# Optimization experiments

Measured on AMD Instinct MI355X. Metric: run time of the kernel, lower is better.

The kernel has to match this reference:

```python
import jax, jax.numpy as jnp
import numpy as np

ATTN_WINDOW = 7  # attention_window from attn_params; dilation (attention_stride) = 1


def _xavier(key, shape):
    lim = np.sqrt(6.0 / (shape[0] + shape[1]))
    return jax.random.uniform(key, shape, jnp.float32, -lim, lim)


def setup_inputs() -> dict:
    key = jax.random.key(0)
    ks = jax.random.split(key, 8)
    B, Cin, Him, Wim = 4, 3, 112, 112
    Cmid, Cout = 128, 128
    x = jax.random.normal(ks[0], (B, Cin, Him, Wim), jnp.float32)
    conv_w = jax.random.normal(ks[1], (Cmid, Cin, 3, 3), jnp.float32) * 0.1  # OIHW
    conv_b = jnp.zeros((Cmid,), jnp.float32)
    q_w = _xavier(ks[2], (Cmid, Cmid)); q_b = jnp.zeros((Cmid,), jnp.float32)
    k_w = _xavier(ks[3], (Cmid, Cmid)); k_b = jnp.zeros((Cmid,), jnp.float32)
    v_w = _xavier(ks[4], (Cout, Cmid)); v_b = jnp.zeros((Cout,), jnp.float32)
    return {"x": x, "conv_w": conv_w, "conv_b": conv_b,
            "q_w": q_w, "q_b": q_b, "k_w": k_w, "k_b": k_b, "v_w": v_w, "v_b": v_b}


def _neighbor_idx(n, ksz):
    # NATTEN-style neighborhood: centered window, clamped to stay inside the image.
    starts = jnp.clip(jnp.arange(n) - ksz // 2, 0, n - ksz)
    return starts[:, None] + jnp.arange(ksz)[None, :]  # [n, ksz]


def reference(x, conv_w, conv_b, q_w, q_b, k_w, k_b, v_w, v_b):
    # conv stem (3x3, stride 2, pad 1) + ReLU
    f = jax.lax.conv_general_dilated(
        x, conv_w, window_strides=(2, 2), padding=[(1, 1), (1, 1)],
        dimension_numbers=("NCHW", "OIHW", "NCHW"))
    f = jax.nn.relu(f + conv_b[None, :, None, None])
    f = f.transpose(0, 2, 3, 1)  # NHWC  [B,H,W,Cmid]
    # 1x1 convs == per-pixel linear layers
    q = f @ q_w.T + q_b
    k = f @ k_w.T + k_b
    v = f @ v_w.T + v_b
    B, H, W, C = q.shape
    ksz = min(ATTN_WINDOW, H, W)
    ksz -= 1 if ksz % 2 == 0 else 0
    ih = _neighbor_idx(H, ksz)  # [H, ksz]
    iw = _neighbor_idx(W, ksz)  # [W, ksz]
    # gather per-pixel neighborhoods: [B,H,W,ksz,ksz,C]
    kn = k[:, ih[:, None, :, None], iw[None, :, None, :], :]
    vn = v[:, ih[:, None, :, None], iw[None, :, None, :], :]
    scale = C ** -0.5
    logits = jnp.einsum("bhwc,bhwijc->bhwij", q * scale, kn)
    attn = jax.nn.softmax(logits.reshape(B, H, W, -1), axis=-1).reshape(logits.shape)
    out = jnp.einsum("bhwij,bhwijc->bhwc", attn, vn)  # [B,H,W,Cout]
    return out.transpose(0, 3, 1, 2)  # back to NCHW
```

## Files before the change

### kernel.cpp

```cpp
#include <hip/hip_runtime.h>
#include <hip/hip_bf16.h>
#include <math.h>

#define HW 56
#define PPI (HW*HW)
#define NB 4
#define C 128
#define NPIX (NB*PPI)

typedef __attribute__((ext_vector_type(8))) short short8;
typedef __attribute__((ext_vector_type(4))) float f32x4;

__device__ __forceinline__ short bfbits(float v) {
    __hip_bfloat16 hb = __float2bfloat16(v);
    return *reinterpret_cast<short*>(&hb);
}
__device__ __forceinline__ unsigned packbf(float a, float b) {
    return (unsigned)(unsigned short)bfbits(a) | ((unsigned)(unsigned short)bfbits(b) << 16);
}

__global__ __launch_bounds__(256) void prep_kernel(
    const float* __restrict__ cw,
    const float* __restrict__ qw, const float* __restrict__ kw,
    const float* __restrict__ vw,
    __hip_bfloat16* __restrict__ wcf, __hip_bfloat16* __restrict__ wqkv)
{
    int gid = blockIdx.x * 256 + threadIdx.x;
    if (blockIdx.x < 192) {
        int m   = gid >> 14;
        int r   = gid & 16383;
        int col = r >> 7;
        int k   = r & 127;
        const float* W = (m == 0) ? qw : (m == 1) ? kw : vw;
        int kk = k >> 5, hi = (k >> 3) & 3, j = k & 7;
        wqkv[m * 16384 + ((kk * 4 + hi) * 128 + col) * 8 + j] = __float2bfloat16(W[col * 128 + k]);
    } else {
        int idx = gid - 192 * 256;
        int hi = idx >> 10, cout = (idx >> 3) & 127, j = idx & 7;
        int k  = hi * 8 + j;
        float v = (k < 27) ? cw[cout * 27 + k] : 0.f;
        wcf[(hi * 128 + cout) * 8 + j] = __float2bfloat16(v);
    }
}

#define VPITCH 272
#define XPITCH 24
#define XCH    504
#define LPITCH 100

__global__ __launch_bounds__(256, 2) void fused_kernel(
    const float* __restrict__ x, const __hip_bfloat16* __restrict__ wcf,
    const float* __restrict__ cb, const __hip_bfloat16* __restrict__ wqkv,
    const float* __restrict__ qb, const float* __restrict__ kb,
    const float* __restrict__ vb, float* __restrict__ out)
{
    __shared__ __align__(16) short vT[128 * 136];
    __shared__ __align__(16) short poolA[4][16 * 128];
    __shared__ __align__(16) short poolB[16 * 136];
    __shared__ __align__(16) float logit_s[16 * LPITCH];
    short* q_lds = poolA[0];
    short* x_lds = poolB;
    short* attnW = poolB;

    int t = threadIdx.x, lane = t & 63, wid = t >> 6;
    int r16 = lane & 15, hi = lane >> 4;

    int bx = blockIdx.x;
    int b  = bx / 196;
    int rr = bx % 196;
    int th = rr / 14, tw = rr % 14;
    int ih0 = min(max(th*4 - 3, 0), HW - 10);
    int iw0 = min(max(tw*4 - 3, 0), HW - 10);

    {
        int ihA = 2*ih0 - 1, iwA = 2*iw0 - 1;
        #pragma unroll
        for (int it = 0; it < 6; ++it) {
            int i = t + 256*it;
            if (i < 1512) {
                int ci = i / XCH, r = i % XCH;
                int row = r / XPITCH, col = r % XPITCH;
                int ih = ihA + row, iw = iwA + col;
                float xv = 0.f;
                if (col < 21 && ih >= 0 && ih < 112 && iw >= 0 && iw < 112)
                    xv = x[((size_t)(b*3 + ci)*112 + ih)*112 + iw];
                x_lds[i] = bfbits(xv);
            }
        }
    }

    for (int i = t; i < 1024; i += 256) {
        int c = i >> 3, j = i & 7;
        int hsw = (c >> 3) & 7;
        int unit = (14 + (j >> 2)) ^ hsw;
        *(unsigned*)((char*)vT + c*VPITCH + (unit << 4) + (j & 3)*4) = 0u;
    }

    int  offb[8];
    bool vmask[8];
    #pragma unroll
    for (int j = 0; j < 8; ++j) {
        int k = hi*8 + j;
        int ci = k/9, r9 = k%9, kh = r9/3, kw_ = r9%3;
        offb[j]  = ci*XCH + kh*XPITCH + kw_;
        vmask[j] = (k < 27);
    }
    float qbias[2];
    #pragma unroll
    for (int i = 0; i < 2; ++i) qbias[i] = qb[(wid*2 + i)*16 + r16];

    __syncthreads();

    short8 qa[4];
    {
        int cout0 = (wid*2 + 0)*16 + r16;
        int cout1 = (wid*2 + 1)*16 + r16;
        short8 cbw0 = *(const short8*)((const short*)wcf + (hi*128 + cout0)*8);
        short8 cbw1 = *(const short8*)((const short*)wcf + (hi*128 + cout1)*8);
        float cbias0 = cb[cout0], cbias1 = cb[cout1];

        int ph = th*4 + (r16 >> 2), pw = tw*4 + (r16 & 3);
        int hl = ph - ih0, wl = pw - iw0;
        int pb = hl*(2*XPITCH) + wl*2;
        short8 af;
        #pragma unroll
        for (int j = 0; j < 8; ++j)
            af[j] = vmask[j] ? x_lds[offb[j] + pb] : (short)0;
        #pragma unroll
        for (int ctl = 0; ctl < 2; ++ctl) {
            int cout   = ctl ? cout1  : cout0;
            short8 bw  = ctl ? cbw1   : cbw0;
            float bias = ctl ? cbias1 : cbias0;
            f32x4 acc = {0.f, 0.f, 0.f, 0.f};
            acc = __builtin_amdgcn_mfma_f32_16x16x32_bf16(af, bw, acc, 0, 0, 0);
            int colblk = cout >> 3, inb = (cout & 7)*2;
            #pragma unroll
            for (int rg = 0; rg < 4; ++rg) {
                int px = hi*4 + rg;
                *(short*)((char*)q_lds + px*256 + ((colblk ^ px) << 4) + inb)
                    = bfbits(fmaxf(acc[rg] + bias, 0.f));
            }
        }
        __syncthreads();

        short8 fa[4];
        #pragma unroll
        for (int kk = 0; kk < 4; ++kk)
            fa[kk] = *(const short8*)((char*)q_lds + r16*256 + (((kk*4 + hi) ^ r16) << 4));

        __syncthreads();

        #pragma unroll
        for (int i = 0; i < 2; ++i) {
            int ct = wid*2 + i;
            const short* wb = (const short*)wqkv + hi*1024 + r16*8 + ct*128;
            f32x4 acc = {0.f, 0.f, 0.f, 0.f};
            acc = __builtin_amdgcn_mfma_f32_16x16x32_bf16(fa[0], *(const short8*)(wb),         acc, 0, 0, 0);
            acc = __builtin_amdgcn_mfma_f32_16x16x32_bf16(fa[1], *(const short8*)(wb +  4096), acc, 0, 0, 0);
            acc = __builtin_amdgcn_mfma_f32_16x16x32_bf16(fa[2], *(const short8*)(wb +  8192), acc, 0, 0, 0);
            acc = __builtin_amdgcn_mfma_f32_16x16x32_bf16(fa[3], *(const short8*)(wb + 12288), acc, 0, 0, 0);
            int c = ct*16 + r16;
            float bb = qbias[i];
            #pragma unroll
            for (int rg = 0; rg < 4; ++rg) {
                int px = hi*4 + rg;
                *(short*)((char*)q_lds + px*256 + (((c >> 3) ^ px) << 4) + (c & 7)*2)
                    = bfbits(acc[rg] + bb);
            }
        }
        __syncthreads();

        #pragma unroll
        for (int kk = 0; kk < 4; ++kk)
            qa[kk] = *(const short8*)((char*)q_lds + r16*256 + (((kk*4 + hi) ^ r16) << 4));
        __syncthreads();
    }

    {
        short* myb = poolA[wid];

        short8 cbw8[8];
        float  cbias8[8], kbias8[8], vbias8[8];
        #pragma unroll
        for (int ct = 0; ct < 8; ++ct) {
            int c = ct*16 + r16;
            cbw8[ct]   = *(const short8*)((const short*)wcf + (hi*128 + c)*8);
            cbias8[ct] = cb[c];
            kbias8[ct] = kb[c];
            vbias8[ct] = vb[c];
        }

        #pragma unroll
        for (int j = 0; j < 2; ++j) {
            int cc = wid + 4*j;
            if (cc < 7) {
                int nc = min(cc*16 + r16, 99);
                int hl = nc/10, wl = nc - 10*hl;
                int pb = hl*(2*XPITCH) + wl*2;
                short8 af;
                #pragma unroll
                for (int j2 = 0; j2 < 8; ++j2)
                    af[j2] = vmask[j2] ? x_lds[offb[j2] + pb] : (short)0;

                #pragma unroll
                for (int ct = 0; ct < 8; ++ct) {
                    f32x4 acc = {0.f, 0.f, 0.f, 0.f};
                    acc = __builtin_amdgcn_mfma_f32_16x16x32_bf16(af, cbw8[ct], acc, 0, 0, 0);
                    int cout = ct*16 + r16;
                    int colblk = cout >> 3, inb = (cout & 7)*2;
                    #pragma unroll
                    for (int rg = 0; rg < 4; ++rg) {
                        int px = hi*4 + rg;
                        *(short*)((char*)myb + px*256 + ((colblk ^ px) << 4) + inb)
                            = bfbits(fmaxf(acc[rg] + cbias8[ct], 0.f));
                    }
                }

                short8 fa[4];
                #pragma unroll
                for (int kk = 0; kk < 4; ++kk)
                    fa[kk] = *(const short8*)((char*)myb + r16*256 + (((kk*4 + hi) ^ r16) << 4));

                #pragma unroll
                for (int ct = 0; ct < 8; ++ct) {
                    const short* wb = (const short*)wqkv + 16384 + hi*1024 + r16*8 + ct*128;
                    f32x4 acc = {0.f, 0.f, 0.f, 0.f};
                    acc = __builtin_amdgcn_mfma_f32_16x16x32_bf16(fa[0], *(const short8*)(wb),         acc, 0, 0, 0);
                    acc = __builtin_amdgcn_mfma_f32_16x16x32_bf16(fa[1], *(const short8*)(wb +  4096), acc, 0, 0, 0);
                    acc = __builtin_amdgcn_mfma_f32_16x16x32_bf16(fa[2], *(const short8*)(wb +  8192), acc, 0, 0, 0);
                    acc = __builtin_amdgcn_mfma_f32_16x16x32_bf16(fa[3], *(const short8*)(wb + 12288), acc, 0, 0, 0);
                    int c = ct*16 + r16;
                    int swz = c >> 3;
                    #pragma unroll
                    for (int rg = 0; rg < 4; ++rg) {
                        int nl = hi*4 + rg;
                        *(short*)((char*)myb + nl*256 + ((swz ^ nl) << 4) + (c & 7)*2)
                            = bfbits(acc[rg] + kbias8[ct]);
                    }
                }

                #pragma unroll
                for (int ct = 0; ct < 8; ++ct) {
                    const short* wb = (const short*)wqkv + 2*16384 + hi*1024 + r16*8 + ct*128;
                    f32x4 acc = {0.f, 0.f, 0.f, 0.f};
                    acc = __builtin_amdgcn_mfma_f32_16x16x32_bf16(fa[0], *(const short8*)(wb),         acc, 0, 0, 0);
                    acc = __builtin_amdgcn_mfma_f32_16x16x32_bf16(fa[1], *(const short8*)(wb +  4096), acc, 0, 0, 0);
                    acc = __builtin_amdgcn_mfma_f32_16x16x32_bf16(fa[2], *(const short8*)(wb +  8192), acc, 0, 0, 0);
                    acc = __builtin_amdgcn_mfma_f32_16x16x32_bf16(fa[3], *(const short8*)(wb + 12288), acc, 0, 0, 0);
                    int c = ct*16 + r16;
                    float bb = vbias8[ct];
                    int n0 = cc*16 + hi*4;
                    unsigned lo  = packbf(acc[0] + bb, acc[1] + bb);
                    unsigned hi2 = packbf(acc[2] + bb, acc[3] + bb);
                    int hsw = (c >> 3) & 7;
                    int off = (2*n0) ^ (hsw << 4);
                    *(uint2*)((char*)vT + c*VPITCH + off) = make_uint2(lo, hi2);
                }

                {
                    const char* kbase = (const char*)myb + r16*256;
                    f32x4 acc = {0.f, 0.f, 0.f, 0.f};
                    #pragma unroll
                    for (int kk = 0; kk < 4; ++kk) {
                        short8 kv = *(const short8*)(kbase + (((kk*4 + hi) ^ r16) << 4));
                        acc = __builtin_amdgcn_mfma_f32_16x16x32_bf16(qa[kk], kv, acc, 0, 0, 0);
                    }
                    int col = cc*16 + r16;
                    if (col < 100) {
                        #pragma unroll
                        for (int rg = 0; rg < 4; ++rg)
                            logit_s[(hi*4 + rg)*LPITCH + col] = acc[rg];
                    }
                }
            }
        }
    }
    __syncthreads();

    {
        unsigned* aw = (unsigned*)attnW;
        for (int i = t; i < 1088; i += 256) aw[i] = 0u;
    }
    __syncthreads();

    {
        int r7 = lane / 7, s7 = lane - 7*r7;
        bool valid = lane < 49;
        const float scale = 0.08838834764831845f;
        #pragma unroll
        for (int px = 0; px < 4; ++px) {
            int p = wid*4 + px;
            int h = th*4 + (p >> 2), w = tw*4 + (p & 3);
            int hs = min(max(h - 3, 0), HW - 7);
            int ws = min(max(w - 3, 0), HW - 7);
            int col = (hs - ih0 + r7)*10 + (ws - iw0 + s7);
            float lg = valid ? logit_s[p*LPITCH + col] * scale : -INFINITY;
            float m = lg;
            #pragma unroll
            for (int d = 1; d < 64; d <<= 1) m = fmaxf(m, __shfl_xor(m, d));
            float e = valid ? __expf(lg - m) : 0.f;
            float s = e;
            #pragma unroll
            for (int d = 1; d < 64; d <<= 1) s += __shfl_xor(s, d);
            if (valid) {
                __hip_bfloat16 hb = __float2bfloat16(e / s);
                *(__hip_bfloat16*)((char*)attnW + p*VPITCH + 2*col) = hb;
            }
        }
    }
    __syncthreads();

    short8 pa[4];
    #pragma unroll
    for (int kk = 0; kk < 4; ++kk)
        pa[kk] = *(const short8*)((char*)attnW + r16*VPITCH + kk*64 + hi*16);

    for (int nt = wid; nt < 8; nt += 4) {
        int c   = nt*16 + r16;
        int hsw = (c >> 3) & 7;
        const char* vrow = (const char*)vT + c*VPITCH;
        f32x4 acc = {0.f, 0.f, 0.f, 0.f};
        #pragma unroll
        for (int kk = 0; kk < 4; ++kk) {
            short8 vbr = *(const short8*)(vrow + ((kk*64 + hi*16) ^ (hsw << 4)));
            acc = __builtin_amdgcn_mfma_f32_16x16x32_bf16(pa[kk], vbr, acc, 0, 0, 0);
        }
        #pragma unroll
        for (int rg = 0; rg < 4; ++rg) {
            int p = hi*4 + rg;
            int h = th*4 + (p >> 2), w = tw*4 + (p & 3);
            out[(((size_t)b*C + c)*HW + h)*HW + w] = acc[rg];
        }
    }
}

extern "C" void kernel_launch(void* const* d_in, const int* in_sizes, int n_in,
                              void* d_out, int out_size, void* d_ws, size_t ws_size,
                              hipStream_t stream) {
    const float* x      = (const float*)d_in[0];
    const float* conv_w = (const float*)d_in[1];
    const float* conv_b = (const float*)d_in[2];
    const float* q_w    = (const float*)d_in[3];
    const float* q_b    = (const float*)d_in[4];
    const float* k_w    = (const float*)d_in[5];
    const float* k_b    = (const float*)d_in[6];
    const float* v_w    = (const float*)d_in[7];
    const float* v_b    = (const float*)d_in[8];
    float* out = (float*)d_out;

    __hip_bfloat16* wqkv = (__hip_bfloat16*)d_ws;
    __hip_bfloat16* wcf  = wqkv + 3 * 16384;

    prep_kernel<<<208, 256, 0, stream>>>(conv_w, q_w, k_w, v_w, wcf, wqkv);
    fused_kernel<<<NB*196, 256, 0, stream>>>(x, wcf, conv_b, wqkv,
                                             q_b, k_b, v_b, out);
}
```

Measured before the change: 43.48 us.

## Write attention output as NHWC scratch and transpose to NCHW in separate kernel

The fused kernel now writes its output in NHWC order to a workspace buffer instead of scattering strided writes into NCHW. A new transpose kernel stages two image rows per block through shared memory and writes coalesced float2 rows into the NCHW output. This is meant to replace the uncoalesced 4-element scattered stores with contiguous writes. In exchange it adds an extra launch and a round trip of the full output (about 6.4 MB) through global memory.

```diff
diff --git a/kernel.cpp b/kernel.cpp
--- a/kernel.cpp
+++ b/kernel.cpp
@@ -52,7 +52,7 @@
     const float* __restrict__ x, const __hip_bfloat16* __restrict__ wcf,
     const float* __restrict__ cb, const __hip_bfloat16* __restrict__ wqkv,
     const float* __restrict__ qb, const float* __restrict__ kb,
-    const float* __restrict__ vb, float* __restrict__ out)
+    const float* __restrict__ vb, float* __restrict__ onh)
 {
     __shared__ __align__(16) short vT[128 * 136];
     __shared__ __align__(16) short poolA[4][16 * 128];
@@ -329,7 +329,39 @@
         for (int rg = 0; rg < 4; ++rg) {
             int p = hi*4 + rg;
             int h = th*4 + (p >> 2), w = tw*4 + (p & 3);
-            out[(((size_t)b*C + c)*HW + h)*HW + w] = acc[rg];
+            onh[(size_t)(b*PPI + h*HW + w)*C + c] = acc[rg];
+        }
+    }
+}
+
+__global__ __launch_bounds__(256) void tr_kernel(
+    const float* __restrict__ onh, float* __restrict__ out)
+{
+    __shared__ float ld[128][113];
+
+    int t = threadIdx.x, lane = t & 63, wid = t >> 6;
+    int blk = blockIdx.x;
+    int b   = blk / 28, h2 = blk % 28;
+    size_t pix0 = (size_t)b * PPI + h2 * 112;
+
+    #pragma unroll
+    for (int k = 0; k < 28; ++k) {
+        int idx = t + 256*k;
+        int p = idx >> 6, c2 = idx & 63;
+        float2 v = *(const float2*)(onh + (pix0 + p)*C + 2*c2);
+        ld[2*c2][p]     = v.x;
+        ld[2*c2 + 1][p] = v.y;
+    }
+    __syncthreads();
+
+    #pragma unroll
+    for (int cc = 0; cc < 32; ++cc) {
+        int c = wid + 4*cc;
+        if (lane < 56) {
+            float2 v;
+            v.x = ld[c][2*lane];
+            v.y = ld[c][2*lane + 1];
+            *(float2*)(out + ((size_t)(b*C + c))*PPI + h2*112 + 2*lane) = v;
         }
     }
 }
@@ -350,8 +382,10 @@
 
     __hip_bfloat16* wqkv = (__hip_bfloat16*)d_ws;
     __hip_bfloat16* wcf  = wqkv + 3 * 16384;
+    float*          onh  = (float*)((char*)d_ws + 106496);
 
     prep_kernel<<<208, 256, 0, stream>>>(conv_w, q_w, k_w, v_w, wcf, wqkv);
     fused_kernel<<<NB*196, 256, 0, stream>>>(x, wcf, conv_b, wqkv,
-                                             q_b, k_b, v_b, out);
-}
+                                             q_b, k_b, v_b, onh);
+    tr_kernel<<<NB*28, 256, 0, stream>>>(onh, out);
+}
```

Result: slower. 45.36 us (+4.3%).
